# Optimization experiments

Hardware: AMD Instinct MI355X
Metric: run time of the kernel (lower is better)

Reference implementation:

```python
import jax, jax.numpy as jnp
import numpy as np

B, N, DIM = 16, 1024, 768
H = 12
HD = DIM // H
SCALE = HD ** -0.5

def setup_inputs() -> dict:
    key = jax.random.key(0)
    k1, k2, k3, k4 = jax.random.split(key, 4)
    x = jax.random.normal(k1, (B, N, DIM), dtype=jnp.float32)
    # qkv: Linear(dim, 3*dim, bias=False); torch weight is [out, in]
    w_qkv = jax.random.normal(k2, (3 * DIM, DIM), dtype=jnp.float32) * (DIM ** -0.5)
    # proj: Linear(dim, dim) with bias
    w_proj = jax.random.normal(k3, (DIM, DIM), dtype=jnp.float32) * (DIM ** -0.5)
    b_proj = jax.random.normal(k4, (DIM,), dtype=jnp.float32) * 0.02
    return {"x": x, "w_qkv": w_qkv, "w_proj": w_proj, "b_proj": b_proj}

def reference(x, w_qkv, w_proj, b_proj):
    B_, N_, D_ = x.shape
    # qkv projection: [B, N, 3*D] -> [3, B, H, N, HD]
    qkv = jnp.einsum('bnd,ed->bne', x, w_qkv)
    qkv = qkv.reshape(B_, N_, 3, H, HD).transpose(2, 0, 3, 1, 4)
    q, k, v = qkv[0], qkv[1], qkv[2]
    # attention scores [B, H, N, N]
    attn = jnp.einsum('bhqd,bhkd->bhqk', q, k) * SCALE
    attn = jax.nn.softmax(attn, axis=-1)
    # weighted values -> [B, N, D]
    out = jnp.einsum('bhqk,bhkd->bhqd', attn, v)
    out = out.transpose(0, 2, 1, 3).reshape(B_, N_, D_)
    # output projection
    out = jnp.einsum('bnd,ed->bne', out, w_proj) + b_proj
    return out
```

## Files before the change

### kernel.cpp

```cpp
#include <hip/hip_runtime.h>
#include <cstdint>

#define B_SZ 16
#define SEQ 1024
#define DIM 768
#define NH 12
#define HD 64
#define M_TOTAL (B_SZ*SEQ)
#define QKV_OUT (3*DIM)
#define EXP2_SCALE 0.18033688011f

typedef _Float16 f16;
typedef __attribute__((ext_vector_type(8))) f16 f16x8;
typedef __attribute__((ext_vector_type(4))) f16 f16x4;
typedef __attribute__((ext_vector_type(2))) __fp16 pk16x2;
typedef __attribute__((ext_vector_type(4))) short s4_t;
typedef __attribute__((ext_vector_type(4))) float f32x4;
typedef unsigned int u32;
typedef const __attribute__((address_space(1))) u32* gas_t;
typedef __attribute__((address_space(3))) u32* las_t;

union U4 { pk16x2 h2[2]; f16x4 v; };
union U8 { pk16x2 h2[4]; f16x8 v; };
union HS { f16 h; short s; };

__device__ __forceinline__ void async16(const void* g, void* l) {
    __builtin_amdgcn_global_load_lds((gas_t)g, (las_t)l, 16, 0, 0);
}
__device__ __forceinline__ f32x4 mfma32h(f16x8 a, f16x8 b, f32x4 c) {
    return __builtin_amdgcn_mfma_f32_16x16x32_f16(a, b, c, 0, 0, 0);
}
__device__ __forceinline__ f16x8 ldfragh(const short* p) {
    return *(const f16x8*)p;
}

__global__ void cvt_kernel(const float* __restrict__ x, const float* __restrict__ wq,
                           const float* __restrict__ wp,
                           short* __restrict__ xb, short* __restrict__ wqb, short* __restrict__ wpb) {
    const long nx = (long)M_TOTAL * DIM / 4;
    const long nq = (long)QKV_OUT * DIM / 4;
    const long np = (long)DIM * DIM / 4;
    const long total = nx + nq + np;
    for (long i = (long)blockIdx.x * blockDim.x + threadIdx.x; i < total;
         i += (long)gridDim.x * blockDim.x) {
        const float4* src; short* dst; long off;
        if (i < nx)            { src = (const float4*)x;  dst = xb;  off = i; }
        else if (i < nx + nq)  { src = (const float4*)wq; dst = wqb; off = i - nx; }
        else                   { src = (const float4*)wp; dst = wpb; off = i - nx - nq; }
        float4 v = src[off];
        U4 u;
        u.h2[0] = __builtin_amdgcn_cvt_pkrtz(v.x, v.y);
        u.h2[1] = __builtin_amdgcn_cvt_pkrtz(v.z, v.w);
        *(f16x4*)(dst + off * 4) = u.v;
    }
}

template<int QM, int QN>
__device__ __forceinline__ void mfma_quad(f32x4 (&acc)[8][4], const f16x8 (&af)[4][2],
                                          const f16x8 (&bf)[4][2]) {
#pragma unroll
    for (int r = 0; r < 4; ++r)
#pragma unroll
        for (int c = 0; c < 2; ++c) {
            f32x4 t = acc[QM * 4 + r][QN * 2 + c];
            t = mfma32h(af[r][0], bf[QN * 2 + c][0], t);
            t = mfma32h(af[r][1], bf[QN * 2 + c][1], t);
            acc[QM * 4 + r][QN * 2 + c] = t;
        }
}

template<int EPI, int N, int K>
__global__ __launch_bounds__(512, 2) void gemm_bt(const short* __restrict__ A,
                                                  const short* __restrict__ Bm,
                                                  short* __restrict__ Cq, short* __restrict__ Ck,
                                                  short* __restrict__ Cv,
                                                  float* __restrict__ Cout,
                                                  const float* __restrict__ bias) {
    static_assert(K % 128 == 0, "even K-tile count required");
    constexpr int NT = K / 64;
    constexpr int NIT = NT / 2;
    __shared__ short lds[65536];

    const int tid = threadIdx.x;
    const int l = tid & 63, quad = l >> 4, l15 = l & 15, l7 = l15 & 7;
    const int w = tid >> 6, wr = w >> 2, wc = w & 3;

    const int gx = gridDim.x;
    const int nwg = gx * (int)gridDim.y;
    int fid = (int)blockIdx.y * gx + (int)blockIdx.x;
    fid = (fid & 7) * (nwg >> 3) + (fid >> 3);
    const int m0 = (fid / gx) * 256;
    const int n0 = (fid % gx) * 256;

    const int srow = tid >> 3, sc = tid & 7;
    const int scc = sc ^ (srow & 7);
    const short* Asrc = A + (size_t)(m0 + srow) * K + scc * 8;
    const short* Bsrc = Bm + (size_t)(n0 + srow) * K + scc * 8;
    const int sdst = srow * 64 + sc * 8;

#define STAGE_A(t, hi) do {                                              \
        const int sb_ = ((t) & 1) * 32768 + (hi) * 8192;                 \
        const size_t go_ = (size_t)((hi) * 128) * K + (size_t)(t) * 64;  \
        async16(Asrc + go_, &lds[sb_ + sdst]);                           \
        async16(Asrc + go_ + (size_t)64 * K, &lds[sb_ + sdst + 4096]);   \
    } while (0)
#define STAGE_B(t, hi) do {                                              \
        const int sb_ = ((t) & 1) * 32768 + 16384 + (hi) * 8192;         \
        const size_t go_ = (size_t)((hi) * 128) * K + (size_t)(t) * 64;  \
        async16(Bsrc + go_, &lds[sb_ + sdst]);                           \
        async16(Bsrc + go_ + (size_t)64 * K, &lds[sb_ + sdst + 4096]);   \
    } while (0)

    const int aoff = wr * 8192 + l15 * 64;
    const int boff = 16384 + wc * 4096 + l15 * 64;
    const int c0 = (quad ^ l7) * 8;
    const int c1 = ((4 + quad) ^ l7) * 8;

#define RD_A(SB, MHALF) do {                                                                  \
        const int ab_ = (SB) + aoff + (MHALF) * 4096;                                         \
        af[0][0] = ldfragh(&lds[ab_ + c0]);        af[0][1] = ldfragh(&lds[ab_ + c1]);        \
        af[1][0] = ldfragh(&lds[ab_ + 1024 + c0]); af[1][1] = ldfragh(&lds[ab_ + 1024 + c1]); \
        af[2][0] = ldfragh(&lds[ab_ + 2048 + c0]); af[2][1] = ldfragh(&lds[ab_ + 2048 + c1]); \
        af[3][0] = ldfragh(&lds[ab_ + 3072 + c0]); af[3][1] = ldfragh(&lds[ab_ + 3072 + c1]); \
    } while (0)
#define RD_B(SB, NHALF) do {                                                                             \
        const int bb_ = (SB) + boff + (NHALF) * 2048;                                                    \
        bf[(NHALF)*2][0]   = ldfragh(&lds[bb_ + c0]);        bf[(NHALF)*2][1]   = ldfragh(&lds[bb_ + c1]);        \
        bf[(NHALF)*2+1][0] = ldfragh(&lds[bb_ + 1024 + c0]); bf[(NHALF)*2+1][1] = ldfragh(&lds[bb_ + 1024 + c1]); \
    } while (0)

#define BAR1() __builtin_amdgcn_s_barrier()
#define BAR2() do { __builtin_amdgcn_s_barrier(); __builtin_amdgcn_sched_barrier(0); } while (0)
#define VMC4() asm volatile("s_waitcnt vmcnt(4)" ::: "memory")
#define VMC0() asm volatile("s_waitcnt vmcnt(0)" ::: "memory")
#define MQ(QM, QN) do {                                        \
        __builtin_amdgcn_s_setprio(1);                         \
        mfma_quad<QM, QN>(acc, af, bf);                        \
        __builtin_amdgcn_s_setprio(0);                         \
    } while (0)

    f32x4 acc[8][4];
#pragma unroll
    for (int i = 0; i < 8; ++i)
#pragma unroll
        for (int j = 0; j < 4; ++j) acc[i][j] = (f32x4){0.f, 0.f, 0.f, 0.f};
    f16x8 af[4][2], bf[4][2];

    STAGE_B(0, 0); STAGE_B(0, 1); STAGE_A(0, 0); STAGE_A(0, 1);
    STAGE_B(1, 0); STAGE_B(1, 1);
    VMC4();
    BAR2();

    for (int i = 0; i < NIT; ++i) {
        const int to = 2 * i + 1, t2 = 2 * i + 2, t3 = 2 * i + 3;
        RD_A(0, 0); RD_B(0, 0);
        STAGE_A(to, 0);
        BAR1(); MQ(0, 0); BAR2();

        RD_B(0, 1);
        STAGE_A(to, 1);
        BAR1(); MQ(0, 1); BAR2();

        RD_A(0, 1);
        if (t2 < NT) STAGE_B(t2, 0);
        BAR1(); MQ(1, 0); BAR2();

        if (t2 < NT) STAGE_B(t2, 1);
        BAR1(); MQ(1, 1);
        if (i == NIT - 1) VMC0(); else VMC4();
        BAR2();

        RD_A(32768, 0); RD_B(32768, 0);
        if (t2 < NT) STAGE_A(t2, 0);
        BAR1(); MQ(0, 0); BAR2();

        RD_B(32768, 1);
        if (t2 < NT) STAGE_A(t2, 1);
        BAR1(); MQ(0, 1); BAR2();

        RD_A(32768, 1);
        if (t3 < NT) STAGE_B(t3, 0);
        BAR1(); MQ(1, 0); BAR2();

        if (t3 < NT) STAGE_B(t3, 1);
        BAR1(); MQ(1, 1);
        if (i == NIT - 1) VMC0(); else VMC4();
        BAR2();
    }
#undef STAGE_A
#undef STAGE_B
#undef RD_A
#undef RD_B

#pragma unroll
    for (int rt = 0; rt < 8; ++rt) {
        const int mrow = m0 + wr * 128 + (rt >> 2) * 64 + (rt & 3) * 16 + quad * 4;
#pragma unroll
        for (int ct = 0; ct < 4; ++ct) {
            const int col = n0 + wc * 64 + (ct >> 1) * 32 + (ct & 1) * 16 + l15;
            if (EPI == 0) {
                int s = col / DIM;
                int h = (col - s * DIM) >> 6, hd = col & 63;
                int b = mrow >> 10, nn = mrow & 1023;
                if (s == 2) {
                    U4 u;
                    u.h2[0] = __builtin_amdgcn_cvt_pkrtz(acc[rt][ct][0], acc[rt][ct][1]);
                    u.h2[1] = __builtin_amdgcn_cvt_pkrtz(acc[rt][ct][2], acc[rt][ct][3]);
                    *(f16x4*)&Cv[(((size_t)b * NH + h) * HD + hd) * SEQ + nn] = u.v;
                } else {
                    short* dst = (s == 0) ? Cq : Ck;
                    const float qs = (s == 0) ? EXP2_SCALE : 1.0f;
#pragma unroll
                    for (int r = 0; r < 4; ++r) {
                        HS t; t.h = (f16)(acc[rt][ct][r] * qs);
                        dst[(((size_t)b * NH + h) * SEQ + nn + r) * HD + hd] = t.s;
                    }
                }
            } else {
                float bv = bias[col];
#pragma unroll
                for (int r = 0; r < 4; ++r)
                    Cout[(size_t)(mrow + r) * N + col] = acc[rt][ct][r] + bv;
            }
        }
    }
}

__global__ __launch_bounds__(256) void attn_kernel(const short* __restrict__ Q,
                                                   const short* __restrict__ Km,
                                                   const short* __restrict__ Vt,
                                                   short* __restrict__ O) {
    __shared__ short lds[4][4096];
    const int tid = threadIdx.x;
    const int w = tid >> 6, l = tid & 63, quad = l >> 4, l15 = l & 15;
    const int bid = blockIdx.x;
    const int xcd = bid & 7, kk = bid >> 3;
    const int head = xcd + 8 * (kk >> 3);
    const int q0 = (kk & 7) * 128 + w * 32;
    const int b = head / NH, h = head - b * NH;
    const short* Qp = Q + (size_t)head * (SEQ * HD);
    const short* Kp = Km + (size_t)head * (SEQ * HD);
    const short* Vp = Vt + (size_t)head * (SEQ * HD);

    f16x8 qf[2][2];
#pragma unroll
    for (int qt = 0; qt < 2; ++qt)
#pragma unroll
        for (int hf = 0; hf < 2; ++hf)
            qf[qt][hf] = *(const f16x8*)&Qp[(q0 + qt * 16 + l15) * HD + hf * 32 + quad * 8];

    f32x4 oacc[2][4];
#pragma unroll
    for (int qt = 0; qt < 2; ++qt)
#pragma unroll
        for (int ht = 0; ht < 4; ++ht) oacc[qt][ht] = (f32x4){0.f, 0.f, 0.f, 0.f};
    float psum[2] = {0.f, 0.f};

    const int kr = tid >> 3, kc = tid & 7;
    const int kcc = kc ^ ((kr & 3) ^ (((kr >> 3) & 3) << 1));
    const short* kSrc = Kp + kr * HD + kcc * 8;
    const int kDst = kr * 64 + kc * 8;
    const int vr = tid >> 2, vc = tid & 3;
    const int vcc = vc ^ ((vr >> 1) & 3);
    const short* vSrc = Vp + vr * SEQ + vcc * 8;
    const int vDst = 2048 + vr * 32 + vc * 8;

#define STAGE(bf, g) do {                                   \
        async16(kSrc + (g) * (32 * HD), &lds[bf][kDst]);    \
        async16(vSrc + (g) * 32, &lds[bf][vDst]);           \
    } while (0)

    const int rA = 8 * (l15 >> 2) + (l15 & 3);
    const int sk = (l15 & 3) ^ ((l15 >> 2) << 1);
    const int offK = rA * 64 + ((quad ^ sk) * 8);
    const int offV = 2048 + l15 * 32 + ((quad ^ ((l15 >> 1) & 3)) * 8);

    STAGE(0, 0); STAGE(1, 1); STAGE(2, 2);

    for (int g = 0; g < 32; ++g) {
        if (g <= 29)      asm volatile("s_waitcnt vmcnt(4)" ::: "memory");
        else if (g == 30) asm volatile("s_waitcnt vmcnt(2)" ::: "memory");
        else              asm volatile("s_waitcnt vmcnt(0)" ::: "memory");
        __builtin_amdgcn_s_barrier();
        if (g < 29) STAGE((g + 3) & 3, g + 3);

        const short* kb = &lds[g & 3][0];
        f16x8 kA0 = ldfragh(kb + offK);
        f16x8 kA1 = ldfragh(kb + (offK ^ 32));
        f16x8 kB0 = ldfragh(kb + offK + 256);
        f16x8 kB1 = ldfragh(kb + (offK ^ 32) + 256);
        f16x8 v0 = ldfragh(kb + offV);
        f16x8 v1 = ldfragh(kb + offV + 512);
        f16x8 v2 = ldfragh(kb + offV + 1024);
        f16x8 v3 = ldfragh(kb + offV + 1536);

        __builtin_amdgcn_s_setprio(1);
#pragma unroll
        for (int qt = 0; qt < 2; ++qt) {
            f32x4 sA = (f32x4){0.f, 0.f, 0.f, 0.f};
            sA = mfma32h(kA0, qf[qt][0], sA);
            sA = mfma32h(kA1, qf[qt][1], sA);
            f32x4 sB = (f32x4){0.f, 0.f, 0.f, 0.f};
            sB = mfma32h(kB0, qf[qt][0], sB);
            sB = mfma32h(kB1, qf[qt][1], sB);
            float eA0 = __builtin_amdgcn_exp2f(sA[0]);
            float eA1 = __builtin_amdgcn_exp2f(sA[1]);
            float eA2 = __builtin_amdgcn_exp2f(sA[2]);
            float eA3 = __builtin_amdgcn_exp2f(sA[3]);
            float eB0 = __builtin_amdgcn_exp2f(sB[0]);
            float eB1 = __builtin_amdgcn_exp2f(sB[1]);
            float eB2 = __builtin_amdgcn_exp2f(sB[2]);
            float eB3 = __builtin_amdgcn_exp2f(sB[3]);
            psum[qt] += ((eA0 + eA1) + (eA2 + eA3)) + ((eB0 + eB1) + (eB2 + eB3));
            U8 u;
            u.h2[0] = __builtin_amdgcn_cvt_pkrtz(eA0, eA1);
            u.h2[1] = __builtin_amdgcn_cvt_pkrtz(eA2, eA3);
            u.h2[2] = __builtin_amdgcn_cvt_pkrtz(eB0, eB1);
            u.h2[3] = __builtin_amdgcn_cvt_pkrtz(eB2, eB3);
            oacc[qt][0] = mfma32h(v0, u.v, oacc[qt][0]);
            oacc[qt][1] = mfma32h(v1, u.v, oacc[qt][1]);
            oacc[qt][2] = mfma32h(v2, u.v, oacc[qt][2]);
            oacc[qt][3] = mfma32h(v3, u.v, oacc[qt][3]);
        }
        __builtin_amdgcn_s_setprio(0);
    }
#undef STAGE

#pragma unroll
    for (int qt = 0; qt < 2; ++qt) {
        psum[qt] += __shfl_xor(psum[qt], 16);
        psum[qt] += __shfl_xor(psum[qt], 32);
    }

#pragma unroll
    for (int qt = 0; qt < 2; ++qt) {
        float rinv = 1.0f / psum[qt];
        short* orow = &O[((size_t)b * SEQ + q0 + qt * 16 + l15) * DIM + h * HD + quad * 4];
#pragma unroll
        for (int ht = 0; ht < 4; ++ht) {
            U4 u;
            u.h2[0] = __builtin_amdgcn_cvt_pkrtz(oacc[qt][ht][0] * rinv, oacc[qt][ht][1] * rinv);
            u.h2[1] = __builtin_amdgcn_cvt_pkrtz(oacc[qt][ht][2] * rinv, oacc[qt][ht][3] * rinv);
            *(f16x4*)(orow + ht * 16) = u.v;
        }
    }
}

extern "C" void kernel_launch(void* const* d_in, const int* in_sizes, int n_in,
                              void* d_out, int out_size, void* d_ws, size_t ws_size,
                              hipStream_t stream) {
    const float* x      = (const float*)d_in[0];
    const float* w_qkv  = (const float*)d_in[1];
    const float* w_proj = (const float*)d_in[2];
    const float* b_proj = (const float*)d_in[3];
    float* out = (float*)d_out;

    short* p = (short*)d_ws;
    short* Xb  = p; p += (size_t)M_TOTAL * DIM;
    short* Wqb = p; p += (size_t)QKV_OUT * DIM;
    short* Wpb = p; p += (size_t)DIM * DIM;
    short* Qb  = p; p += (size_t)B_SZ * NH * SEQ * HD;
    short* Kb  = p; p += (size_t)B_SZ * NH * SEQ * HD;
    short* Vtb = p; p += (size_t)B_SZ * NH * SEQ * HD;
    short* Ob  = p; p += (size_t)M_TOTAL * DIM;

    cvt_kernel<<<1024, 256, 0, stream>>>(x, w_qkv, w_proj, Xb, Wqb, Wpb);
    gemm_bt<0, QKV_OUT, DIM><<<dim3(QKV_OUT / 256, M_TOTAL / 256), 512, 0, stream>>>(
        Xb, Wqb, Qb, Kb, Vtb, nullptr, nullptr);
    attn_kernel<<<B_SZ * NH * (SEQ / 128), 256, 0, stream>>>(Qb, Kb, Vtb, Ob);
    gemm_bt<1, DIM, DIM><<<dim3(DIM / 256, M_TOTAL / 256), 512, 0, stream>>>(
        Ob, Wpb, nullptr, nullptr, nullptr, out, b_proj);
}
```

Baseline: 273.6 us.

## Halve GEMM K-tile with new LDS swizzle and double attention queries per wave

```diff
diff --git a/kernel.cpp b/kernel.cpp
--- a/kernel.cpp
+++ b/kernel.cpp
@@ -56,17 +56,13 @@
 }
 
 template<int QM, int QN>
-__device__ __forceinline__ void mfma_quad(f32x4 (&acc)[8][4], const f16x8 (&af)[4][2],
-                                          const f16x8 (&bf)[4][2]) {
+__device__ __forceinline__ void mfma_quad(f32x4 (&acc)[8][4], const f16x8 (&af)[4],
+                                          const f16x8 (&bf)[4]) {
 #pragma unroll
     for (int r = 0; r < 4; ++r)
 #pragma unroll
-        for (int c = 0; c < 2; ++c) {
-            f32x4 t = acc[QM * 4 + r][QN * 2 + c];
-            t = mfma32h(af[r][0], bf[QN * 2 + c][0], t);
-            t = mfma32h(af[r][1], bf[QN * 2 + c][1], t);
-            acc[QM * 4 + r][QN * 2 + c] = t;
-        }
+        for (int c = 0; c < 2; ++c)
+            acc[QM * 4 + r][QN * 2 + c] = mfma32h(af[r], bf[QN * 2 + c], acc[QM * 4 + r][QN * 2 + c]);
 }
 
 template<int EPI, int N, int K>
@@ -76,14 +72,15 @@
                                                   short* __restrict__ Cv,
                                                   float* __restrict__ Cout,
                                                   const float* __restrict__ bias) {
-    static_assert(K % 128 == 0, "even K-tile count required");
-    constexpr int NT = K / 64;
+    static_assert(K % 64 == 0, "even K-tile count required");
+    constexpr int NT = K / 32;
     constexpr int NIT = NT / 2;
-    __shared__ short lds[65536];
+    __shared__ short lds[32768];
 
     const int tid = threadIdx.x;
-    const int l = tid & 63, quad = l >> 4, l15 = l & 15, l7 = l15 & 7;
+    const int l = tid & 63, quad = l >> 4, l15 = l & 15;
     const int w = tid >> 6, wr = w >> 2, wc = w & 3;
+    const int fl = (l15 & 3) ^ ((l15 >> 2) & 3);
 
     const int gx = gridDim.x;
     const int nwg = gx * (int)gridDim.y;
@@ -92,46 +89,37 @@
     const int m0 = (fid / gx) * 256;
     const int n0 = (fid % gx) * 256;
 
-    const int srow = tid >> 3, sc = tid & 7;
-    const int scc = sc ^ (srow & 7);
+    const int srow = tid >> 2, sc = tid & 3;
+    const int scc = sc ^ ((srow & 3) ^ ((srow >> 2) & 3));
     const short* Asrc = A + (size_t)(m0 + srow) * K + scc * 8;
     const short* Bsrc = Bm + (size_t)(n0 + srow) * K + scc * 8;
-    const int sdst = srow * 64 + sc * 8;
-
-#define STAGE_A(t, hi) do {                                              \
-        const int sb_ = ((t) & 1) * 32768 + (hi) * 8192;                 \
-        const size_t go_ = (size_t)((hi) * 128) * K + (size_t)(t) * 64;  \
-        async16(Asrc + go_, &lds[sb_ + sdst]);                           \
-        async16(Asrc + go_ + (size_t)64 * K, &lds[sb_ + sdst + 4096]);   \
+    const int sdst = srow * 32 + sc * 8;
+
+#define STAGE_A(t, hi) async16(Asrc + (size_t)((hi) * 128) * K + (t) * 32, \
+                               &lds[((t) & 1) * 16384 + (hi) * 4096 + sdst])
+#define STAGE_B(t, hi) async16(Bsrc + (size_t)((hi) * 128) * K + (t) * 32, \
+                               &lds[((t) & 1) * 16384 + 8192 + (hi) * 4096 + sdst])
+
+    const int aoff = wr * 4096 + l15 * 32;
+    const int boff = 8192 + wc * 2048 + l15 * 32;
+    const int c0 = (quad ^ fl) * 8;
+
+#define RD_A(SB, MH) do {                                  \
+        const int ab_ = (SB) + aoff + (MH) * 2048;         \
+        af[0] = ldfragh(&lds[ab_ + c0]);                   \
+        af[1] = ldfragh(&lds[ab_ + 512 + c0]);             \
+        af[2] = ldfragh(&lds[ab_ + 1024 + c0]);            \
+        af[3] = ldfragh(&lds[ab_ + 1536 + c0]);            \
     } while (0)
-#define STAGE_B(t, hi) do {                                              \
-        const int sb_ = ((t) & 1) * 32768 + 16384 + (hi) * 8192;         \
-        const size_t go_ = (size_t)((hi) * 128) * K + (size_t)(t) * 64;  \
-        async16(Bsrc + go_, &lds[sb_ + sdst]);                           \
-        async16(Bsrc + go_ + (size_t)64 * K, &lds[sb_ + sdst + 4096]);   \
-    } while (0)
-
-    const int aoff = wr * 8192 + l15 * 64;
-    const int boff = 16384 + wc * 4096 + l15 * 64;
-    const int c0 = (quad ^ l7) * 8;
-    const int c1 = ((4 + quad) ^ l7) * 8;
-
-#define RD_A(SB, MHALF) do {                                                                  \
-        const int ab_ = (SB) + aoff + (MHALF) * 4096;                                         \
-        af[0][0] = ldfragh(&lds[ab_ + c0]);        af[0][1] = ldfragh(&lds[ab_ + c1]);        \
-        af[1][0] = ldfragh(&lds[ab_ + 1024 + c0]); af[1][1] = ldfragh(&lds[ab_ + 1024 + c1]); \
-        af[2][0] = ldfragh(&lds[ab_ + 2048 + c0]); af[2][1] = ldfragh(&lds[ab_ + 2048 + c1]); \
-        af[3][0] = ldfragh(&lds[ab_ + 3072 + c0]); af[3][1] = ldfragh(&lds[ab_ + 3072 + c1]); \
-    } while (0)
-#define RD_B(SB, NHALF) do {                                                                             \
-        const int bb_ = (SB) + boff + (NHALF) * 2048;                                                    \
-        bf[(NHALF)*2][0]   = ldfragh(&lds[bb_ + c0]);        bf[(NHALF)*2][1]   = ldfragh(&lds[bb_ + c1]);        \
-        bf[(NHALF)*2+1][0] = ldfragh(&lds[bb_ + 1024 + c0]); bf[(NHALF)*2+1][1] = ldfragh(&lds[bb_ + 1024 + c1]); \
+#define RD_B(SB, NH) do {                                  \
+        const int bb_ = (SB) + boff + (NH) * 1024;         \
+        bf[(NH) * 2]     = ldfragh(&lds[bb_ + c0]);        \
+        bf[(NH) * 2 + 1] = ldfragh(&lds[bb_ + 512 + c0]);  \
     } while (0)
 
 #define BAR1() __builtin_amdgcn_s_barrier()
 #define BAR2() do { __builtin_amdgcn_s_barrier(); __builtin_amdgcn_sched_barrier(0); } while (0)
-#define VMC4() asm volatile("s_waitcnt vmcnt(4)" ::: "memory")
+#define VMC2() asm volatile("s_waitcnt vmcnt(2)" ::: "memory")
 #define VMC0() asm volatile("s_waitcnt vmcnt(0)" ::: "memory")
 #define MQ(QM, QN) do {                                        \
         __builtin_amdgcn_s_setprio(1);                         \
@@ -144,11 +132,11 @@
     for (int i = 0; i < 8; ++i)
 #pragma unroll
         for (int j = 0; j < 4; ++j) acc[i][j] = (f32x4){0.f, 0.f, 0.f, 0.f};
-    f16x8 af[4][2], bf[4][2];
+    f16x8 af[4], bf[4];
 
     STAGE_B(0, 0); STAGE_B(0, 1); STAGE_A(0, 0); STAGE_A(0, 1);
     STAGE_B(1, 0); STAGE_B(1, 1);
-    VMC4();
+    VMC2();
     BAR2();
 
     for (int i = 0; i < NIT; ++i) {
@@ -167,24 +155,24 @@
 
         if (t2 < NT) STAGE_B(t2, 1);
         BAR1(); MQ(1, 1);
-        if (i == NIT - 1) VMC0(); else VMC4();
+        if (i == NIT - 1) VMC0(); else VMC2();
         BAR2();
 
-        RD_A(32768, 0); RD_B(32768, 0);
+        RD_A(16384, 0); RD_B(16384, 0);
         if (t2 < NT) STAGE_A(t2, 0);
         BAR1(); MQ(0, 0); BAR2();
 
-        RD_B(32768, 1);
+        RD_B(16384, 1);
         if (t2 < NT) STAGE_A(t2, 1);
         BAR1(); MQ(0, 1); BAR2();
 
-        RD_A(32768, 1);
+        RD_A(16384, 1);
         if (t3 < NT) STAGE_B(t3, 0);
         BAR1(); MQ(1, 0); BAR2();
 
         if (t3 < NT) STAGE_B(t3, 1);
         BAR1(); MQ(1, 1);
-        if (i == NIT - 1) VMC0(); else VMC4();
+        if (i == NIT - 1) VMC0(); else VMC2();
         BAR2();
     }
 #undef STAGE_A
@@ -235,26 +223,26 @@
     const int w = tid >> 6, l = tid & 63, quad = l >> 4, l15 = l & 15;
     const int bid = blockIdx.x;
     const int xcd = bid & 7, kk = bid >> 3;
-    const int head = xcd + 8 * (kk >> 3);
-    const int q0 = (kk & 7) * 128 + w * 32;
+    const int head = xcd + 8 * (kk >> 2);
+    const int q0 = (kk & 3) * 256 + w * 64;
     const int b = head / NH, h = head - b * NH;
     const short* Qp = Q + (size_t)head * (SEQ * HD);
     const short* Kp = Km + (size_t)head * (SEQ * HD);
     const short* Vp = Vt + (size_t)head * (SEQ * HD);
 
-    f16x8 qf[2][2];
-#pragma unroll
-    for (int qt = 0; qt < 2; ++qt)
+    f16x8 qf[4][2];
+#pragma unroll
+    for (int qt = 0; qt < 4; ++qt)
 #pragma unroll
         for (int hf = 0; hf < 2; ++hf)
             qf[qt][hf] = *(const f16x8*)&Qp[(q0 + qt * 16 + l15) * HD + hf * 32 + quad * 8];
 
-    f32x4 oacc[2][4];
-#pragma unroll
-    for (int qt = 0; qt < 2; ++qt)
+    f32x4 oacc[4][4];
+#pragma unroll
+    for (int qt = 0; qt < 4; ++qt)
 #pragma unroll
         for (int ht = 0; ht < 4; ++ht) oacc[qt][ht] = (f32x4){0.f, 0.f, 0.f, 0.f};
-    float psum[2] = {0.f, 0.f};
+    float psum[4] = {0.f, 0.f, 0.f, 0.f};
 
     const int kr = tid >> 3, kc = tid & 7;
     const int kcc = kc ^ ((kr & 3) ^ (((kr >> 3) & 3) << 1));
@@ -296,7 +284,7 @@
 
         __builtin_amdgcn_s_setprio(1);
 #pragma unroll
-        for (int qt = 0; qt < 2; ++qt) {
+        for (int qt = 0; qt < 4; ++qt) {
             f32x4 sA = (f32x4){0.f, 0.f, 0.f, 0.f};
             sA = mfma32h(kA0, qf[qt][0], sA);
             sA = mfma32h(kA1, qf[qt][1], sA);
@@ -327,13 +315,13 @@
 #undef STAGE
 
 #pragma unroll
-    for (int qt = 0; qt < 2; ++qt) {
+    for (int qt = 0; qt < 4; ++qt) {
         psum[qt] += __shfl_xor(psum[qt], 16);
         psum[qt] += __shfl_xor(psum[qt], 32);
     }
 
 #pragma unroll
-    for (int qt = 0; qt < 2; ++qt) {
+    for (int qt = 0; qt < 4; ++qt) {
         float rinv = 1.0f / psum[qt];
         short* orow = &O[((size_t)b * SEQ + q0 + qt * 16 + l15) * DIM + h * HD + quad * 4];
 #pragma unroll
@@ -367,7 +355,7 @@
     cvt_kernel<<<1024, 256, 0, stream>>>(x, w_qkv, w_proj, Xb, Wqb, Wpb);
     gemm_bt<0, QKV_OUT, DIM><<<dim3(QKV_OUT / 256, M_TOTAL / 256), 512, 0, stream>>>(
         Xb, Wqb, Qb, Kb, Vtb, nullptr, nullptr);
-    attn_kernel<<<B_SZ * NH * (SEQ / 128), 256, 0, stream>>>(Qb, Kb, Vtb, Ob);
+    attn_kernel<<<B_SZ * NH * (SEQ / 256), 256, 0, stream>>>(Qb, Kb, Vtb, Ob);
     gemm_bt<1, DIM, DIM><<<dim3(DIM / 256, M_TOTAL / 256), 512, 0, stream>>>(
         Ob, Wpb, nullptr, nullptr, nullptr, out, b_proj);
 }
```

Result: slower. 282.5 us (+3.3%).
